# Optimization experiments

Hardware: AMD Instinct MI355X
Metric: run time of the kernel (lower is better)

The kernel has to match this reference:

```python
import jax, jax.numpy as jnp
import numpy as np

N = 50000        # n_nodes
E = 1_600_000    # n_edges (avg degree 32)
IN = 128         # in_dim
H = 8            # num_heads
R = 16           # hidden_rank
D = 16           # out_dim (per head)
SCALE = float(np.sqrt(D))


def setup_inputs() -> dict:
    key = jax.random.key(0)
    k1, k2, k3, k4, k5, k6 = jax.random.split(key, 6)
    h = jax.random.normal(k1, (N, IN), jnp.float32)
    src = jax.random.randint(k2, (E,), 0, N, dtype=jnp.int32)
    dst = jax.random.randint(k3, (E,), 0, N, dtype=jnp.int32)
    s = 1.0 / np.sqrt(IN)  # kaiming-ish scale
    p = jax.random.normal(k4, (IN, H * R), jnp.float32) * s
    q = jax.random.normal(k5, (IN, H * R), jnp.float32) * s
    Wv = jax.random.normal(k6, (IN, H * D), jnp.float32) * s
    return {"h": h, "src": src, "dst": dst, "p": p, "q": q, "Wv": Wv}


def reference(h, src, dst, p, q, Wv):
    # global_attention_type == 'transform' -> atted = h
    K = (h @ q).reshape(N, H, R)   # K_h = atted @ _q
    Q = (h @ p).reshape(N, H, R)   # Q_h = h @ _p
    V = (h @ Wv).reshape(N, H, D)  # V_h = V(h), no bias
    # per-edge score: (K[src] * Q[dst]).sum(-1, keepdim), then scaled exp
    score = jnp.sum(K[src] * Q[dst], axis=-1, keepdims=True)   # [E, H, 1]
    score = jnp.exp(jnp.clip(score / SCALE, -5.0, 5.0))
    # scatter-sum into destination nodes
    wV = jax.ops.segment_sum(V[src] * score, dst, num_segments=N)  # [N, H, D]
    z = jax.ops.segment_sum(score, dst, num_segments=N)            # [N, H, 1]
    z = jnp.where(z == 0, jnp.float32(0.001), z)
    return wV / z
```

## Files before the change

kernel.cpp:

```cpp
#include <hip/hip_runtime.h>
#include <hip/hip_fp16.h>


#define HNODE 64
#define EPB   4096
#define BKT_SHIFT 7
#define BKT_CAP 5120

typedef _Float16 f16x8 __attribute__((ext_vector_type(8)));
typedef float    f32x4 __attribute__((ext_vector_type(4)));
typedef _Float16 hv2   __attribute__((ext_vector_type(2)));

__device__ __forceinline__ float fdot2(unsigned a, unsigned b, float c) {
#if __has_builtin(__builtin_amdgcn_fdot2)
    return __builtin_amdgcn_fdot2(__builtin_bit_cast(hv2, a),
                                  __builtin_bit_cast(hv2, b), c, false);
#else
    __half2 ah = *(__half2*)&a, bh = *(__half2*)&b;
    float2 af = __half22float2(ah), bf = __half22float2(bh);
    return c + af.x * bf.x + af.y * bf.y;
#endif
}

__device__ __forceinline__ float2 h2f(unsigned u) {
    __half2 hh = *(__half2*)&u;
    return __half22float2(hh);
}

__device__ __forceinline__ unsigned pack2(float a, float b) {
    __half2 hh = __floats2half2_rn(a, b);
    return *(unsigned*)&hh;
}

__device__ __forceinline__ float clamp5(float x) {
#if __has_builtin(__builtin_amdgcn_fmed3f)
    return __builtin_amdgcn_fmed3f(x, -5.f, 5.f);
#else
    return fminf(fmaxf(x, -5.f), 5.f);
#endif
}

#if __has_builtin(__builtin_amdgcn_mov_dpp)
#define QBCAST(v, J) __builtin_amdgcn_mov_dpp((v), (J) * 0x55, 0xF, 0xF, true)
__device__ __forceinline__ float qadd_xor1(float x) {
    int y = __builtin_amdgcn_mov_dpp(__float_as_int(x), 0xB1, 0xF, 0xF, true);
    return x + __int_as_float(y);
}
__device__ __forceinline__ float qadd_xor2(float x) {
    int y = __builtin_amdgcn_mov_dpp(__float_as_int(x), 0x4E, 0xF, 0xF, true);
    return x + __int_as_float(y);
}
#else
#define QBCAST(v, J) __shfl((v), ((threadIdx.x & 63) & ~3) + (J), 64)
__device__ __forceinline__ float qadd_xor1(float x) { return x + __shfl_xor(x, 1); }
__device__ __forceinline__ float qadd_xor2(float x) { return x + __shfl_xor(x, 2); }
#endif

__global__ __launch_bounds__(256) void wt_convert_kernel(
    const float* __restrict__ Wq, const float* __restrict__ Wp,
    const float* __restrict__ Wv, __half* __restrict__ Wt,
    int* __restrict__ btot, int nbkt)
{
    int o = blockIdx.x * 256 + threadIdx.x;
    if (o < 49152) {
        int m = o >> 14, rem = o & 16383;
        int nn = rem >> 7, kk = rem & 127;
        const float* W = (m == 0) ? Wq : (m == 1) ? Wp : Wv;
        Wt[o] = __float2half(W[kk * 128 + nn]);
    } else {
        int i = o - 49152;
        if (i < nbkt) btot[i] = 0;
    }
}

__global__ __launch_bounds__(256) void gemm_scatter_kernel(
    const float* __restrict__ h, const __half* __restrict__ Wt,
    unsigned* __restrict__ KV, __half* __restrict__ Q, int n,
    const int* __restrict__ src, const int* __restrict__ dst,
    unsigned* __restrict__ gcsr, int* __restrict__ btot,
    int E, int nbkt, int gemm_blocks)
{
    __shared__ __align__(16) char smem[39936];
    const int t = threadIdx.x;

    if ((int)blockIdx.x < gemm_blocks) {
        _Float16* ws = (_Float16*)smem;
        const int wid = t >> 6, lane = t & 63;
        const int node0 = blockIdx.x * HNODE;
        const int mrow = lane & 15, quad = lane >> 4;

        const int row = node0 + wid * 16 + mrow;
        const bool rowvalid = (row < n);
        const int rowc = rowvalid ? row : (n - 1);

        f16x8 hfr[4];
        #pragma unroll
        for (int s = 0; s < 4; s++) {
            const float4* hp = (const float4*)(h + (size_t)rowc * 128 + quad * 8 + 32 * s);
            float4 f0 = hp[0], f1 = hp[1];
            f16x8 a;
            a[0] = (_Float16)f0.x; a[1] = (_Float16)f0.y;
            a[2] = (_Float16)f0.z; a[3] = (_Float16)f0.w;
            a[4] = (_Float16)f1.x; a[5] = (_Float16)f1.y;
            a[6] = (_Float16)f1.z; a[7] = (_Float16)f1.w;
            hfr[s] = a;
        }

        f32x4 acc[3][8];
        #pragma unroll
        for (int m = 0; m < 3; m++)
            #pragma unroll
            for (int ct = 0; ct < 8; ct++) acc[m][ct] = (f32x4){0.f, 0.f, 0.f, 0.f};

        #pragma unroll
        for (int m = 0; m < 3; m++) {
            __syncthreads();
            {
                const uint4* wg = (const uint4*)(Wt + (size_t)m * 16384);
                #pragma unroll
                for (int i = 0; i < 8; i++) {
                    int idx = t * 8 + i;
                    int r = idx >> 4, seg = idx & 15;
                    *(uint4*)(ws + r * 136 + seg * 8) = wg[idx];
                }
            }
            __syncthreads();
            #pragma unroll
            for (int s = 0; s < 4; s++) {
                #pragma unroll
                for (int ct = 0; ct < 8; ct++) {
                    f16x8 a = *(const f16x8*)(ws + (ct * 16 + mrow) * 136 + quad * 8 + 32 * s);
                    acc[m][ct] = __builtin_amdgcn_mfma_f32_16x16x32_f16(a, hfr[s], acc[m][ct], 0, 0, 0);
                }
            }
        }

        if (rowvalid) {
            #pragma unroll
            for (int ct = 0; ct < 8; ct++) {
                uint4 ov;
                ov.x = pack2(acc[0][ct][0], acc[0][ct][1]);
                ov.y = pack2(acc[0][ct][2], acc[0][ct][3]);
                ov.z = pack2(acc[2][ct][0], acc[2][ct][1]);
                ov.w = pack2(acc[2][ct][2], acc[2][ct][3]);
                *(uint4*)(KV + (((size_t)ct * n + row) << 4) + 4 * quad) = ov;
                uint2 qv;
                qv.x = pack2(acc[1][ct][0], acc[1][ct][1]);
                qv.y = pack2(acc[1][ct][2], acc[1][ct][3]);
                *(uint2*)(Q + (((size_t)ct * n + row) << 4) + 4 * quad) = qv;
            }
        }
    } else {
        unsigned long long* sorted = (unsigned long long*)smem;
        int* cnt  = (int*)(smem + 32768);
        int* lofs = (int*)(smem + 34816);
        int* ts   = (int*)(smem + 36864);
        int* base_sh = (int*)(smem + 37888);

        int blk = blockIdx.x - gemm_blocks;
        for (int i = t; i < 512; i += 256) cnt[i] = 0;
        __syncthreads();

        int4 sv[4], dv[4], rk[4];
        int base = blk * EPB + t * 4;
        #pragma unroll
        for (int r = 0; r < 4; r++) {
            int i = base + r * 1024;
            if (i + 3 < E) {
                sv[r] = *(const int4*)(src + i);
                dv[r] = *(const int4*)(dst + i);
            } else {
                int tsrc[4], tdst[4];
                for (int k = 0; k < 4; k++) {
                    int j = i + k;
                    tsrc[k] = (j < E) ? src[j] : 0;
                    tdst[k] = (j < E) ? dst[j] : -1;
                }
                sv[r] = make_int4(tsrc[0], tsrc[1], tsrc[2], tsrc[3]);
                dv[r] = make_int4(tdst[0], tdst[1], tdst[2], tdst[3]);
            }
            rk[r].x = (dv[r].x >= 0) ? atomicAdd(&cnt[dv[r].x >> BKT_SHIFT], 1) : 0;
            rk[r].y = (dv[r].y >= 0) ? atomicAdd(&cnt[dv[r].y >> BKT_SHIFT], 1) : 0;
            rk[r].z = (dv[r].z >= 0) ? atomicAdd(&cnt[dv[r].z >> BKT_SHIFT], 1) : 0;
            rk[r].w = (dv[r].w >= 0) ? atomicAdd(&cnt[dv[r].w >> BKT_SHIFT], 1) : 0;
        }
        __syncthreads();

        int c0 = cnt[2 * t], c1 = cnt[2 * t + 1];
        int ps = c0 + c1;
        ts[t] = ps; __syncthreads();
        for (int off = 1; off < 256; off <<= 1) {
            int x = ts[t];
            int y = (t >= off) ? ts[t - off] : 0;
            __syncthreads();
            ts[t] = x + y;
            __syncthreads();
        }
        int pbase = ts[t] - ps;
        lofs[2 * t] = pbase;
        lofs[2 * t + 1] = pbase + c0;

        for (int i = t; i < nbkt; i += 256) {
            int c = cnt[i];
            base_sh[i] = (c > 0) ? atomicAdd(&btot[i], c) : 0;
        }
        __syncthreads();

        #pragma unroll
        for (int r = 0; r < 4; r++) {
            int s, d;
            d = dv[r].x; if (d >= 0) { s = sv[r].x; sorted[lofs[d >> BKT_SHIFT] + rk[r].x] = ((unsigned long long)d << 18) | (unsigned)s; }
            d = dv[r].y; if (d >= 0) { s = sv[r].y; sorted[lofs[d >> BKT_SHIFT] + rk[r].y] = ((unsigned long long)d << 18) | (unsigned)s; }
            d = dv[r].z; if (d >= 0) { s = sv[r].z; sorted[lofs[d >> BKT_SHIFT] + rk[r].z] = ((unsigned long long)d << 18) | (unsigned)s; }
            d = dv[r].w; if (d >= 0) { s = sv[r].w; sorted[lofs[d >> BKT_SHIFT] + rk[r].w] = ((unsigned long long)d << 18) | (unsigned)s; }
        }
        __syncthreads();

        int tot = ts[255];
        #pragma unroll
        for (int j = 0; j < 16; j++) {
            int i = j * 256 + t;
            if (i < tot) {
                unsigned long long e = sorted[i];
                int d = (int)(e >> 18);
                int b = d >> BKT_SHIFT;
                int k = i - lofs[b];
                int pos = base_sh[b] + k;
                if (pos < BKT_CAP)
                    gcsr[(size_t)b * BKT_CAP + pos] =
                        ((unsigned)(d & 127) << 18) | (unsigned)(e & 0x3FFFFu);
            }
        }
    }
}

__global__ __launch_bounds__(512) void fine2_kernel(
    const unsigned* __restrict__ gcsr, const int* __restrict__ btot,
    int2* __restrict__ offs, unsigned short* __restrict__ csr,
    int* __restrict__ nodeord, int N)
{
    __shared__ unsigned sedge[BKT_CAP];
    __shared__ unsigned short srank[BKT_CAP];
    __shared__ unsigned short lcsr[BKT_CAP];
    __shared__ int ldeg[128];
    __shared__ int lstart[128];
    __shared__ int ts[128];

    const int b = blockIdx.x, t = threadIdx.x;
    const int seg0 = b * BKT_CAP;

    int tot = btot[b];
    if (tot > BKT_CAP) tot = BKT_CAP;

    if (t < 128) ldeg[t] = 0;
    __syncthreads();

    const unsigned* gb = gcsr + (size_t)b * BKT_CAP;
    for (int i = t; i < tot; i += 512) {
        unsigned w = gb[i];
        sedge[i] = w;
        srank[i] = (unsigned short)atomicAdd(&ldeg[w >> 18], 1);
    }
    __syncthreads();

    int mydeg = (t < 128) ? ldeg[t] : 0;
    if (t < 128) ts[t] = mydeg;
    __syncthreads();
    for (int off = 1; off < 128; off <<= 1) {
        int x = (t < 128) ? ts[t] : 0;
        int y = (t >= off && t < 128) ? ts[t - off] : 0;
        __syncthreads();
        if (t < 128) ts[t] = x + y;
        __syncthreads();
    }
    if (t < 128) {
        int lbeg = ts[t] - mydeg;
        lstart[t] = lbeg;
        int node = (b << 7) + t;
        if (node < N) offs[node] = make_int2(seg0 + lbeg, seg0 + lbeg + mydeg);
        int r = 0;
        for (int j = 0; j < 128; j++) {
            int dj = ldeg[j];
            r += (int)((dj > mydeg) || (dj == mydeg && j < t));
        }
        nodeord[(b << 7) + r] = t;
    }
    __syncthreads();

    for (int i = t; i < tot; i += 512) {
        unsigned w = sedge[i];
        lcsr[lstart[w >> 18] + srank[i]] = (unsigned short)(w & 0x3FFFFu);
    }
    __syncthreads();

    for (int i = t; i < tot; i += 512)
        csr[seg0 + i] = lcsr[i];
}

#define AGG_COMPUTE(A, J)                                                      \
    {                                                                          \
        float s = fdot2(A.x, qq.x, fdot2(A.y, qq.y, 0.f));                     \
        s = qadd_xor1(s);                                                      \
        s = qadd_xor2(s);                                                      \
        float xx = clamp5(s * 0.25f);                                          \
        float sc = (e + (J) < cnt) ? __expf(xx) : 0.f;                         \
        accz += sc;                                                            \
        float2 v0 = h2f(A.z), v1 = h2f(A.w);                                   \
        av0 += sc * v0.x; av1 += sc * v0.y;                                    \
        av2 += sc * v1.x; av3 += sc * v1.y;                                    \
    }

__global__ __launch_bounds__(256) void aggregate_kernel(
    const unsigned* __restrict__ KVh,
    const uint2* __restrict__ Qr,
    const int2* __restrict__ offs, const unsigned short* __restrict__ csr,
    const int* __restrict__ nodeord,
    float* __restrict__ out, int n)
{
    const int t = threadIdx.x;
    const int head = blockIdx.x & 7;
    const int rest = blockIdx.x >> 3;
    const int bkt = rest >> 1, sub = rest & 1;
    const int lane = t & 63;
    const int g = lane >> 2;
    const int p = lane & 3;
    const int chunk = ((t >> 6) << 1) | sub;

    const int spos = (bkt << 7) + (chunk << 4) + g;
    const int local = nodeord[spos];
    const int node = (bkt << 7) + local;
    const bool nvalid = (node < n);
    const int nodec = nvalid ? node : 0;

    int beg = 0, cnt = 0;
    if (nvalid) {
        int2 be = offs[node];
        beg = be.x; cnt = be.y - be.x;
    }

    const size_t hn = (size_t)head * n;
    const uint2 qq = Qr[(hn + nodec) * 4 + p];
    const char* kvb = (const char*)KVh + hn * 64;
    const unsigned ppo = (unsigned)p << 4;

    float accz = 0.f;
    float av0 = 0.f, av1 = 0.f, av2 = 0.f, av3 = 0.f;

    const int cl = (cnt > 0) ? (cnt - 1) : 0;

    int np = (p < cl) ? p : cl;
    int idxA = (int)csr[beg + np];
    uint4 a0, a1, a2, a3;
    {
        unsigned j;
        j = (unsigned)QBCAST(idxA, 0); a0 = *(const uint4*)(kvb + ((j << 6) | ppo));
        j = (unsigned)QBCAST(idxA, 1); a1 = *(const uint4*)(kvb + ((j << 6) | ppo));
        j = (unsigned)QBCAST(idxA, 2); a2 = *(const uint4*)(kvb + ((j << 6) | ppo));
        j = (unsigned)QBCAST(idxA, 3); a3 = *(const uint4*)(kvb + ((j << 6) | ppo));
    }
    np = 4 + p; np = (np < cl) ? np : cl;
    int idxB = (int)csr[beg + np];

    for (int e = 0; e < cnt; e += 4) {
        unsigned j;
        uint4 b0, b1, b2, b3;
        j = (unsigned)QBCAST(idxB, 0); b0 = *(const uint4*)(kvb + ((j << 6) | ppo));
        j = (unsigned)QBCAST(idxB, 1); b1 = *(const uint4*)(kvb + ((j << 6) | ppo));
        j = (unsigned)QBCAST(idxB, 2); b2 = *(const uint4*)(kvb + ((j << 6) | ppo));
        j = (unsigned)QBCAST(idxB, 3); b3 = *(const uint4*)(kvb + ((j << 6) | ppo));
        np = e + 8 + p; np = (np < cl) ? np : cl;
        idxB = (int)csr[beg + np];

        AGG_COMPUTE(a0, 0)
        AGG_COMPUTE(a1, 1)
        AGG_COMPUTE(a2, 2)
        AGG_COMPUTE(a3, 3)

        a0 = b0; a1 = b1; a2 = b2; a3 = b3;
    }

    if (nvalid) {
        float z = accz;
        if (z == 0.f) z = 0.001f;
        float inv = 1.0f / z;
        *(float4*)(out + (size_t)node * 128 + head * 16 + p * 4) =
            make_float4(av0 * inv, av1 * inv, av2 * inv, av3 * inv);
    }
}


extern "C" void kernel_launch(void* const* d_in, const int* in_sizes, int n_in,
                              void* d_out, int out_size, void* d_ws, size_t ws_size,
                              hipStream_t stream)
{
    const float* h   = (const float*)d_in[0];
    const int*   src = (const int*)d_in[1];
    const int*   dst = (const int*)d_in[2];
    const float* p   = (const float*)d_in[3];
    const float* q   = (const float*)d_in[4];
    const float* wv  = (const float*)d_in[5];
    float* out = (float*)d_out;

    const int N = in_sizes[0] / 128;
    const int E = in_sizes[1];
    const int nbkt = (N + 127) >> BKT_SHIFT;
    const int nblk_e = (E + EPB - 1) / EPB;
    const int gemm_blocks = (N + HNODE - 1) / HNODE;

    unsigned* KV = (unsigned*)d_ws;
    __half* Qh   = (__half*)(KV + (size_t)N * 128);
    unsigned* gcsr = (unsigned*)(Qh + (size_t)N * 128);
    int* btot    = (int*)(gcsr + (size_t)nbkt * BKT_CAP);
    unsigned short* csr16 = (unsigned short*)(btot + 512);
    int2* offs   = (int2*)(csr16 + (size_t)nbkt * BKT_CAP);
    int* nodeord = (int*)(offs + N);
    __half* Wt   = (__half*)(nodeord + (size_t)nbkt * 128);

    wt_convert_kernel<<<194, 256, 0, stream>>>(q, p, wv, Wt, btot, nbkt);

    gemm_scatter_kernel<<<gemm_blocks + nblk_e, 256, 0, stream>>>(
        h, Wt, KV, Qh, N, src, dst, gcsr, btot, E, nbkt, gemm_blocks);

    fine2_kernel<<<nbkt, 512, 0, stream>>>(gcsr, btot, offs, csr16, nodeord, N);

    aggregate_kernel<<<nbkt * 16, 256, 0, stream>>>(
        KV, (const uint2*)Qh, offs, csr16, nodeord, (float*)out, N);
}
```

Baseline: 214.4 us.

## Drop LDS local sort in edge bucketing and simplify fine CSR build

The edge-scatter blocks now write each edge straight to its global bucket slot, using the per-block atomic rank. This removes the shared-memory prefix scan and local sort stage, and each block now handles twice as many edges. The fine2 kernel drops its large shared staging arrays, runs with 256 threads, and places edges with per-node atomic cursors while re-reading the bucket from global memory. The GEMM path also prefetches half of the next weight matrix into registers to overlap that load with MFMA work. The trade-offs are less coalesced global writes, a second global read of each bucket, and a nondeterministic edge order within each node.

```diff
diff --git a/kernel.cpp b/kernel.cpp
--- a/kernel.cpp
+++ b/kernel.cpp
@@ -3,7 +3,7 @@
 
 
 #define HNODE 64
-#define EPB   4096
+#define EPB   8192
 #define BKT_SHIFT 7
 #define BKT_CAP 5120
 
@@ -80,7 +80,7 @@
     unsigned* __restrict__ gcsr, int* __restrict__ btot,
     int E, int nbkt, int gemm_blocks)
 {
-    __shared__ __align__(16) char smem[39936];
+    __shared__ __align__(16) char smem[34816];
     const int t = threadIdx.x;
 
     if ((int)blockIdx.x < gemm_blocks) {
@@ -112,19 +112,37 @@
             #pragma unroll
             for (int ct = 0; ct < 8; ct++) acc[m][ct] = (f32x4){0.f, 0.f, 0.f, 0.f};
 
+        uint4 wpre[4];
+        {
+            const uint4* wg = (const uint4*)Wt;
+            #pragma unroll
+            for (int i = 0; i < 4; i++) wpre[i] = wg[t * 8 + i];
+        }
+
         #pragma unroll
         for (int m = 0; m < 3; m++) {
+            const uint4* wg = (const uint4*)(Wt + (size_t)m * 16384);
             __syncthreads();
             {
-                const uint4* wg = (const uint4*)(Wt + (size_t)m * 16384);
                 #pragma unroll
-                for (int i = 0; i < 8; i++) {
+                for (int i = 0; i < 4; i++) {
+                    int idx = t * 8 + i;
+                    int r = idx >> 4, seg = idx & 15;
+                    *(uint4*)(ws + r * 136 + seg * 8) = wpre[i];
+                }
+                #pragma unroll
+                for (int i = 4; i < 8; i++) {
                     int idx = t * 8 + i;
                     int r = idx >> 4, seg = idx & 15;
                     *(uint4*)(ws + r * 136 + seg * 8) = wg[idx];
                 }
             }
             __syncthreads();
+            if (m < 2) {
+                const uint4* wn = (const uint4*)(Wt + (size_t)(m + 1) * 16384);
+                #pragma unroll
+                for (int i = 0; i < 4; i++) wpre[i] = wn[t * 8 + i];
+            }
             #pragma unroll
             for (int s = 0; s < 4; s++) {
                 #pragma unroll
@@ -151,20 +169,17 @@
             }
         }
     } else {
-        unsigned long long* sorted = (unsigned long long*)smem;
-        int* cnt  = (int*)(smem + 32768);
-        int* lofs = (int*)(smem + 34816);
-        int* ts   = (int*)(smem + 36864);
-        int* base_sh = (int*)(smem + 37888);
+        int* cnt     = (int*)smem;
+        int* base_sh = (int*)(smem + 2048);
 
         int blk = blockIdx.x - gemm_blocks;
         for (int i = t; i < 512; i += 256) cnt[i] = 0;
         __syncthreads();
 
-        int4 sv[4], dv[4], rk[4];
+        int4 sv[8], dv[8], rk[8];
         int base = blk * EPB + t * 4;
         #pragma unroll
-        for (int r = 0; r < 4; r++) {
+        for (int r = 0; r < 8; r++) {
             int i = base + r * 1024;
             if (i + 3 < E) {
                 sv[r] = *(const int4*)(src + i);
@@ -186,20 +201,6 @@
         }
         __syncthreads();
 
-        int c0 = cnt[2 * t], c1 = cnt[2 * t + 1];
-        int ps = c0 + c1;
-        ts[t] = ps; __syncthreads();
-        for (int off = 1; off < 256; off <<= 1) {
-            int x = ts[t];
-            int y = (t >= off) ? ts[t - off] : 0;
-            __syncthreads();
-            ts[t] = x + y;
-            __syncthreads();
-        }
-        int pbase = ts[t] - ps;
-        lofs[2 * t] = pbase;
-        lofs[2 * t + 1] = pbase + c0;
-
         for (int i = t; i < nbkt; i += 256) {
             int c = cnt[i];
             base_sh[i] = (c > 0) ? atomicAdd(&btot[i], c) : 0;
@@ -207,43 +208,23 @@
         __syncthreads();
 
         #pragma unroll
-        for (int r = 0; r < 4; r++) {
-            int s, d;
-            d = dv[r].x; if (d >= 0) { s = sv[r].x; sorted[lofs[d >> BKT_SHIFT] + rk[r].x] = ((unsigned long long)d << 18) | (unsigned)s; }
-            d = dv[r].y; if (d >= 0) { s = sv[r].y; sorted[lofs[d >> BKT_SHIFT] + rk[r].y] = ((unsigned long long)d << 18) | (unsigned)s; }
-            d = dv[r].z; if (d >= 0) { s = sv[r].z; sorted[lofs[d >> BKT_SHIFT] + rk[r].z] = ((unsigned long long)d << 18) | (unsigned)s; }
-            d = dv[r].w; if (d >= 0) { s = sv[r].w; sorted[lofs[d >> BKT_SHIFT] + rk[r].w] = ((unsigned long long)d << 18) | (unsigned)s; }
-        }
-        __syncthreads();
-
-        int tot = ts[255];
-        #pragma unroll
-        for (int j = 0; j < 16; j++) {
-            int i = j * 256 + t;
-            if (i < tot) {
-                unsigned long long e = sorted[i];
-                int d = (int)(e >> 18);
-                int b = d >> BKT_SHIFT;
-                int k = i - lofs[b];
-                int pos = base_sh[b] + k;
-                if (pos < BKT_CAP)
-                    gcsr[(size_t)b * BKT_CAP + pos] =
-                        ((unsigned)(d & 127) << 18) | (unsigned)(e & 0x3FFFFu);
-            }
-        }
-    }
-}
-
-__global__ __launch_bounds__(512) void fine2_kernel(
+        for (int r = 0; r < 8; r++) {
+            int s, d, bb, pos;
+            d = dv[r].x; if (d >= 0) { s = sv[r].x; bb = d >> BKT_SHIFT; pos = base_sh[bb] + rk[r].x; if (pos < BKT_CAP) gcsr[(size_t)bb * BKT_CAP + pos] = ((unsigned)(d & 127) << 18) | (unsigned)s; }
+            d = dv[r].y; if (d >= 0) { s = sv[r].y; bb = d >> BKT_SHIFT; pos = base_sh[bb] + rk[r].y; if (pos < BKT_CAP) gcsr[(size_t)bb * BKT_CAP + pos] = ((unsigned)(d & 127) << 18) | (unsigned)s; }
+            d = dv[r].z; if (d >= 0) { s = sv[r].z; bb = d >> BKT_SHIFT; pos = base_sh[bb] + rk[r].z; if (pos < BKT_CAP) gcsr[(size_t)bb * BKT_CAP + pos] = ((unsigned)(d & 127) << 18) | (unsigned)s; }
+            d = dv[r].w; if (d >= 0) { s = sv[r].w; bb = d >> BKT_SHIFT; pos = base_sh[bb] + rk[r].w; if (pos < BKT_CAP) gcsr[(size_t)bb * BKT_CAP + pos] = ((unsigned)(d & 127) << 18) | (unsigned)s; }
+        }
+    }
+}
+
+__global__ __launch_bounds__(256) void fine2_kernel(
     const unsigned* __restrict__ gcsr, const int* __restrict__ btot,
     int2* __restrict__ offs, unsigned short* __restrict__ csr,
     int* __restrict__ nodeord, int N)
 {
-    __shared__ unsigned sedge[BKT_CAP];
-    __shared__ unsigned short srank[BKT_CAP];
-    __shared__ unsigned short lcsr[BKT_CAP];
     __shared__ int ldeg[128];
-    __shared__ int lstart[128];
+    __shared__ int lcur[128];
     __shared__ int ts[128];
 
     const int b = blockIdx.x, t = threadIdx.x;
@@ -256,11 +237,8 @@
     __syncthreads();
 
     const unsigned* gb = gcsr + (size_t)b * BKT_CAP;
-    for (int i = t; i < tot; i += 512) {
-        unsigned w = gb[i];
-        sedge[i] = w;
-        srank[i] = (unsigned short)atomicAdd(&ldeg[w >> 18], 1);
-    }
+    for (int i = t; i < tot; i += 256)
+        atomicAdd(&ldeg[gb[i] >> 18], 1);
     __syncthreads();
 
     int mydeg = (t < 128) ? ldeg[t] : 0;
@@ -275,7 +253,7 @@
     }
     if (t < 128) {
         int lbeg = ts[t] - mydeg;
-        lstart[t] = lbeg;
+        lcur[t] = lbeg;
         int node = (b << 7) + t;
         if (node < N) offs[node] = make_int2(seg0 + lbeg, seg0 + lbeg + mydeg);
         int r = 0;
@@ -287,14 +265,11 @@
     }
     __syncthreads();
 
-    for (int i = t; i < tot; i += 512) {
-        unsigned w = sedge[i];
-        lcsr[lstart[w >> 18] + srank[i]] = (unsigned short)(w & 0x3FFFFu);
-    }
-    __syncthreads();
-
-    for (int i = t; i < tot; i += 512)
-        csr[seg0 + i] = lcsr[i];
+    for (int i = t; i < tot; i += 256) {
+        unsigned w = gb[i];
+        int pos = atomicAdd(&lcur[w >> 18], 1);
+        csr[seg0 + pos] = (unsigned short)(w & 0xFFFFu);
+    }
 }
 
 #define AGG_COMPUTE(A, J)                                                      \
@@ -421,7 +396,7 @@
     gemm_scatter_kernel<<<gemm_blocks + nblk_e, 256, 0, stream>>>(
         h, Wt, KV, Qh, N, src, dst, gcsr, btot, E, nbkt, gemm_blocks);
 
-    fine2_kernel<<<nbkt, 512, 0, stream>>>(gcsr, btot, offs, csr16, nodeord, N);
+    fine2_kernel<<<nbkt, 256, 0, stream>>>(gcsr, btot, offs, csr16, nodeord, N);
 
     aggregate_kernel<<<nbkt * 16, 256, 0, stream>>>(
         KV, (const uint2*)Qh, offs, csr16, nodeord, (float*)out, N);
```

After: 232.5 us. 1.08x slower.
